# Kernel optimization log

Hardware: AMD Instinct MI355X
Metric: run time of the kernel (lower is better)

## Reference

```python
import jax, jax.numpy as jnp
import numpy as np

B, T = 512, 200
N_SKILLS, M, DK, DV, H = 1000, 50, 64, 64, 128


def setup_inputs() -> dict:
    key = jax.random.key(0)
    ks = jax.random.split(key, 12)
    inp = {
        'skill_seq': jax.random.randint(ks[0], (B, T), 0, N_SKILLS, dtype=jnp.int32),
        'correct_seq': jax.random.randint(ks[1], (B, T), 0, 2, dtype=jnp.int32),
        'mask': jnp.ones((B, T), dtype=jnp.float32),
        'skill_embed': jax.random.normal(ks[2], (N_SKILLS, DK), dtype=jnp.float32),
        'key_memory': jax.random.normal(ks[3], (M, DK), dtype=jnp.float32) * 0.1,
        'value_init': jnp.zeros((M, DV), dtype=jnp.float32),
        'interaction_embed': jax.random.normal(ks[4], (2 * N_SKILLS, DV), dtype=jnp.float32),
        'erase_W': jax.random.normal(ks[5], (DV, DV), dtype=jnp.float32) * 0.05,
        'erase_b': jnp.zeros((DV,), dtype=jnp.float32),
        'add_W': jax.random.normal(ks[6], (DV, DV), dtype=jnp.float32) * 0.05,
        'add_b': jnp.zeros((DV,), dtype=jnp.float32),
        'fc1_W': jax.random.normal(ks[7], (DK + DV, H), dtype=jnp.float32) * 0.05,
        'fc1_b': jnp.zeros((H,), dtype=jnp.float32),
        'fc2_W': jax.random.normal(ks[8], (H, 1), dtype=jnp.float32) * 0.05,
        'fc2_b': jnp.zeros((1,), dtype=jnp.float32),
    }
    return inp


def reference(skill_seq, correct_seq, mask, skill_embed, key_memory, value_init,
              interaction_embed, erase_W, erase_b, add_W, add_b,
              fc1_W, fc1_b, fc2_W, fc2_b):
    n_skills = skill_embed.shape[0]
    b = skill_seq.shape[0]
    # Time-invariant-per-step quantities are precomputed vectorized over (B,T):
    q = skill_embed[skill_seq]                                   # (B,T,dk)
    w = jax.nn.softmax(jnp.einsum('btk,mk->btm', q, key_memory), axis=-1)  # (B,T,M)
    v = interaction_embed[skill_seq + correct_seq * n_skills]    # (B,T,dv)
    e = jax.nn.sigmoid(v @ erase_W + erase_b)                    # (B,T,dv)
    a = jnp.tanh(v @ add_W + add_b)                              # (B,T,dv)

    def step(mem, inputs):
        # mem: (B,M,dv); read BEFORE write, matching the torch loop
        w_t, e_t, a_t = inputs                                   # (B,M),(B,dv),(B,dv)
        read = jnp.einsum('bm,bmv->bv', w_t, mem)                # (B,dv)
        we = w_t[:, :, None]                                     # (B,M,1)
        mem = mem * (1.0 - we * e_t[:, None, :]) + we * a_t[:, None, :]
        return mem, read

    mem0 = jnp.broadcast_to(value_init, (b,) + value_init.shape)
    _, reads = jax.lax.scan(step, mem0,
                            (jnp.swapaxes(w, 0, 1), jnp.swapaxes(e, 0, 1), jnp.swapaxes(a, 0, 1)))
    reads = jnp.swapaxes(reads, 0, 1)                            # (B,T,dv)

    x = jnp.concatenate([q, reads], axis=-1)                     # (B,T,dk+dv)
    h = jax.nn.relu(x @ fc1_W + fc1_b)
    logit = (h @ fc2_W + fc2_b)[..., 0]
    p = jax.nn.sigmoid(logit)
    return p * mask, correct_seq.astype(jnp.float32) * mask
```

## Files before the change

kernel.cpp:

```cpp
#include <hip/hip_runtime.h>
#include <hip/hip_bf16.h>

#define B_  512
#define T_  200
#define NS  1000
#define M_  50
#define DK  64
#define DV  64
#define H_  128
#define NPOS (B_ * T_)

typedef __hip_bfloat16 bf16;
typedef unsigned short ushort_t;
typedef __bf16 bf16x8 __attribute__((ext_vector_type(8)));
typedef float  f32x4  __attribute__((ext_vector_type(4)));

__device__ __forceinline__ float ldf(const void* p, int i, int isbf) {
    return isbf ? __bfloat162float(((const bf16*)p)[i]) : ((const float*)p)[i];
}
__device__ __forceinline__ int sniff(const void* mask) {
    return (*(const unsigned*)mask == 0x3F800000u) ? 0 : 1;
}
__device__ __forceinline__ float rl(float x, int l) {
    return __int_as_float(__builtin_amdgcn_readlane(__float_as_int(x), l));
}
__device__ __forceinline__ ushort_t f2bf(float v) {
    bf16 h = __float2bfloat16(v);
    return *(ushort_t*)&h;
}

__global__ __launch_bounds__(256) void dk32_tabs(
    const int*  __restrict__ cseq,
    const void* __restrict__ mask,
    const void* __restrict__ skill_embed, const void* __restrict__ key_memory,
    const void* __restrict__ inter,
    const void* __restrict__ eW, const void* __restrict__ eb,
    const void* __restrict__ aW, const void* __restrict__ ab,
    const void* __restrict__ fc1W, const void* __restrict__ fc1b,
    float* __restrict__ w_tab, unsigned* __restrict__ ea_tab,
    float* __restrict__ hq2, ushort_t* __restrict__ W2f,
    float* __restrict__ out1) {
    int isbf = sniff(mask);
    int lane = threadIdx.x & 63;
    int gwid = (blockIdx.x << 2) | (threadIdx.x >> 6);

    if (gwid < NS) {
        int s = gwid;
        float q = ldf(skill_embed, s * DK + lane, isbf);
        float acc = 0.f;
        if (lane < M_) {
            #pragma unroll 16
            for (int k = 0; k < DK; ++k)
                acc = fmaf(rl(q, k), ldf(key_memory, lane * DK + k, isbf), acc);
        }
        float val = (lane < M_) ? acc : -1e30f;
        float mx = val;
        #pragma unroll
        for (int off = 1; off < 64; off <<= 1) mx = fmaxf(mx, __shfl_xor(mx, off, 64));
        float ex = (lane < M_) ? __expf(val - mx) : 0.f;
        float sm = ex;
        #pragma unroll
        for (int off = 1; off < 64; off <<= 1) sm += __shfl_xor(sm, off, 64);
        w_tab[s * 64 + lane] = (lane < M_) ? ex / sm : 0.f;
    } else if (gwid < 3 * NS) {
        int r = gwid - NS;
        float vv = ldf(inter, r * DV + lane, isbf);
        float eacc = ldf(eb, lane, isbf);
        float aacc = ldf(ab, lane, isbf);
        #pragma unroll 16
        for (int u = 0; u < DV; ++u) {
            float vu = rl(vv, u);
            eacc = fmaf(vu, ldf(eW, u * DV + lane, isbf), eacc);
            aacc = fmaf(vu, ldf(aW, u * DV + lane, isbf), aacc);
        }
        float ev = 1.f / (1.f + __expf(-eacc));
        float av = tanhf(aacc);
        ea_tab[r * 64 + lane] = ((unsigned)f2bf(av) << 16) | (unsigned)f2bf(ev);
    } else if (gwid < 4 * NS) {
        int s = gwid - 3 * NS;
        float q = ldf(skill_embed, s * DK + lane, isbf);
        float acc0 = ldf(fc1b, lane, isbf);
        float acc1 = ldf(fc1b, 64 + lane, isbf);
        #pragma unroll 16
        for (int k = 0; k < DK; ++k) {
            float qk = rl(q, k);
            acc0 = fmaf(qk, ldf(fc1W, k * H_ + lane, isbf), acc0);
            acc1 = fmaf(qk, ldf(fc1W, k * H_ + 64 + lane, isbf), acc1);
        }
        hq2[s * H_ + (lane & 15) * 8 +     (lane >> 4)] = acc0;
        hq2[s * H_ + (lane & 15) * 8 + 4 + (lane >> 4)] = acc1;
    } else if (gwid < 4 * NS + 16) {
        int f = gwid - 4 * NS;
        int tile = f >> 1, kk = f & 1;
        int n = tile * 16 + (lane & 15);
        #pragma unroll
        for (int j = 0; j < 8; ++j) {
            int v = kk * 32 + (lane >> 4) * 8 + j;
            W2f[(f * 64 + lane) * 8 + j] = f2bf(ldf(fc1W, (DK + v) * H_ + n, isbf));
        }
    } else if (gwid < 4 * NS + 16 + 400) {
        int qp = gwid - (4 * NS + 16);
        int t0 = qp * 256;
        #pragma unroll
        for (int i = 0; i < 4; ++i) {
            int idx = t0 + i * 64 + lane;
            out1[idx] = (float)cseq[idx] * ldf(mask, idx, isbf);
        }
    }
}


#define FSCROW(W, MEM) \
    acc0 = fmaf(W.x, MEM.x, acc0); \
    acc1 = fmaf(W.y, MEM.y, acc1); \
    acc2 = fmaf(W.z, MEM.z, acc2); \
    acc3 = fmaf(W.w, MEM.w, acc3); \
    MEM.x = fmaf(-W.x, fmaf(e0, MEM.x, -a0), MEM.x); \
    MEM.y = fmaf(-W.y, fmaf(e0, MEM.y, -a0), MEM.y); \
    MEM.z = fmaf(-W.z, fmaf(e0, MEM.z, -a0), MEM.z); \
    MEM.w = fmaf(-W.w, fmaf(e0, MEM.w, -a0), MEM.w);

#define FSTEP(EAR, WARR, TP, TT) { \
    float e0 = __uint_as_float(EAR << 16); \
    float a0 = __uint_as_float(EAR & 0xFFFF0000u); \
    float acc0 = 0.f, acc1 = 0.f, acc2 = 0.f, acc3 = 0.f; \
    FSCROW(WARR[0], mem[0]) FSCROW(WARR[1], mem[1]) \
    FSCROW(WARR[2], mem[2]) FSCROW(WARR[3], mem[3]) \
    rbf[buf * 4096 + (TP) * 256 + (((k << 6) | lane) ^ (((TP) & 7) << 3))] = \
        f2bf((acc0 + acc1) + (acc2 + acc3)); \
    EAR = ea_tab[(s2 + c2 * NS) * 64 + lane]; \
    WARR[0] = w4[s2 * 16 + 4 * k + 0]; \
    WARR[1] = w4[s2 * 16 + 4 * k + 1]; \
    WARR[2] = w4[s2 * 16 + 4 * k + 2]; \
    WARR[3] = w4[s2 * 16 + 4 * k + 3]; \
    s2 = s3; c2 = c3; \
    { int tf = (TT) + 4; tf = tf < T_ ? tf : T_ - 1; \
      s3 = ss[base + tf]; c3 = cs[base + tf]; } }

__global__ __launch_bounds__(256, 2) void dk32_fused(
    const int*  __restrict__ ss, const int* __restrict__ cs,
    const void* __restrict__ mask, const void* __restrict__ value_init,
    const float* __restrict__ w_tab, const unsigned* __restrict__ ea_tab,
    const float* __restrict__ hq2, const ushort_t* __restrict__ W2f,
    const void* __restrict__ fc2W, const void* __restrict__ fc2b,
    float* __restrict__ out0) {

    __shared__ ushort_t rb[2][16][256];
    __shared__ float    xs[2][4][16];

    int isbf = sniff(mask);
    int lane = threadIdx.x & 63;
    int k    = threadIdx.x >> 6;
    int b    = blockIdx.x;
    const int base = b * T_;
    const float4* w4 = (const float4*)w_tab;
    int col = lane & 15, quad = lane >> 4;
    ushort_t* rbf = &rb[0][0][0];

    const bf16x8* B8 = (const bf16x8*)W2f;
    bf16x8 bA0 = B8[(2 * (2 * k)    ) * 64 + lane];
    bf16x8 bA1 = B8[(2 * (2 * k) + 1) * 64 + lane];
    bf16x8 bB0 = B8[(2 * (2 * k + 1)    ) * 64 + lane];
    bf16x8 bB1 = B8[(2 * (2 * k + 1) + 1) * 64 + lane];
    float f2wA = ldf(fc2W, (2 * k)     * 16 + col, isbf);
    float f2wB = ldf(fc2W, (2 * k + 1) * 16 + col, isbf);
    float f2b  = ldf(fc2b, 0, isbf);

    float4 mem[4];
    #pragma unroll
    for (int i = 0; i < 4; ++i) {
        int r = 16 * k + 4 * i;
        mem[i].x = (r + 0 < M_) ? ldf(value_init, (r + 0) * DV + lane, isbf) : 0.f;
        mem[i].y = (r + 1 < M_) ? ldf(value_init, (r + 1) * DV + lane, isbf) : 0.f;
        mem[i].z = (r + 2 < M_) ? ldf(value_init, (r + 2) * DV + lane, isbf) : 0.f;
        mem[i].w = (r + 3 < M_) ? ldf(value_init, (r + 3) * DV + lane, isbf) : 0.f;
    }

    int s2 = ss[base + 2], c2 = cs[base + 2];
    int s3 = ss[base + 3], c3 = cs[base + 3];

    float4 wa[4], wb[4];
    unsigned eaA, eaB;
    {
        int sA = ss[base], cA = cs[base];
        eaA = ea_tab[(sA + cA * NS) * 64 + lane];
        #pragma unroll
        for (int i = 0; i < 4; ++i) wa[i] = w4[sA * 16 + 4 * k + i];
        int sB = ss[base + 1], cB = cs[base + 1];
        eaB = ea_tab[(sB + cB * NS) * 64 + lane];
        #pragma unroll
        for (int i = 0; i < 4; ++i) wb[i] = w4[sB * 16 + 4 * k + i];
    }

    for (int cc = 0; cc < 13; ++cc) {
        int buf   = cc & 1;
        int p0    = cc * 16;

        FSTEP(eaA, wa, 0, p0 + 0) FSTEP(eaB, wb, 1, p0 + 1)

        int pA = p0 + quad * 4;
        int i0 = pA + 0 < T_ ? pA + 0 : T_ - 1;
        int i1 = pA + 1 < T_ ? pA + 1 : T_ - 1;
        int i2 = pA + 2 < T_ ? pA + 2 : T_ - 1;
        int i3 = pA + 3 < T_ ? pA + 3 : T_ - 1;
        int sp0 = ss[base + i0], sp1 = ss[base + i1];
        int sp2 = ss[base + i2], sp3 = ss[base + i3];

        FSTEP(eaA, wa, 2, p0 + 2) FSTEP(eaB, wb, 3, p0 + 3)

        float2 h0 = *(const float2*)(hq2 + sp0 * H_ + col * 8 + 2 * k);
        float2 h1 = *(const float2*)(hq2 + sp1 * H_ + col * 8 + 2 * k);
        float2 h2 = *(const float2*)(hq2 + sp2 * H_ + col * 8 + 2 * k);
        float2 h3 = *(const float2*)(hq2 + sp3 * H_ + col * 8 + 2 * k);

        FSTEP(eaA, wa, 4, p0 + 4) FSTEP(eaB, wb, 5, p0 + 5)
        FSTEP(eaA, wa, 6, p0 + 6) FSTEP(eaB, wb, 7, p0 + 7)
        if (cc != 12) {
            FSTEP(eaA, wa,  8, p0 +  8) FSTEP(eaB, wb,  9, p0 +  9)
            FSTEP(eaA, wa, 10, p0 + 10) FSTEP(eaB, wb, 11, p0 + 11)
            FSTEP(eaA, wa, 12, p0 + 12) FSTEP(eaB, wb, 13, p0 + 13)
            FSTEP(eaA, wa, 14, p0 + 14) FSTEP(eaB, wb, 15, p0 + 15)
        }
        __syncthreads();

        if (cc > 0 && k == 0 && lane < 16) {
            int p = base + (cc - 1) * 16 + lane;
            float xsum = xs[buf ^ 1][0][lane] + xs[buf ^ 1][1][lane]
                       + xs[buf ^ 1][2][lane] + xs[buf ^ 1][3][lane] + f2b;
            out0[p] = ldf(mask, p, isbf) / (1.f + __expf(-xsum));
        }

        {
            f32x4 cA = {0.f, 0.f, 0.f, 0.f}, cB = {0.f, 0.f, 0.f, 0.f};
            const bf16x8* A8 = (const bf16x8*)&rb[buf][0][0];
            #pragma unroll
            for (int kk = 0; kk < 8; ++kk) {
                bf16x8 av = A8[(col * 32 + kk * 4 + quad) ^ (col & 7)];
                if (kk & 1) {
                    cA = __builtin_amdgcn_mfma_f32_16x16x32_bf16(av, bA1, cA, 0, 0, 0);
                    cB = __builtin_amdgcn_mfma_f32_16x16x32_bf16(av, bB1, cB, 0, 0, 0);
                } else {
                    cA = __builtin_amdgcn_mfma_f32_16x16x32_bf16(av, bA0, cA, 0, 0, 0);
                    cB = __builtin_amdgcn_mfma_f32_16x16x32_bf16(av, bB0, cB, 0, 0, 0);
                }
            }
            float x0, x1, x2, x3, h;
            h = cA.x + h0.x; x0  = fmaxf(h, 0.f) * f2wA;
            h = cB.x + h0.y; x0 += fmaxf(h, 0.f) * f2wB;
            h = cA.y + h1.x; x1  = fmaxf(h, 0.f) * f2wA;
            h = cB.y + h1.y; x1 += fmaxf(h, 0.f) * f2wB;
            h = cA.z + h2.x; x2  = fmaxf(h, 0.f) * f2wA;
            h = cB.z + h2.y; x2 += fmaxf(h, 0.f) * f2wB;
            h = cA.w + h3.x; x3  = fmaxf(h, 0.f) * f2wA;
            h = cB.w + h3.y; x3 += fmaxf(h, 0.f) * f2wB;
            #pragma unroll
            for (int off = 1; off < 16; off <<= 1) {
                x0 += __shfl_xor(x0, off, 64);
                x1 += __shfl_xor(x1, off, 64);
                x2 += __shfl_xor(x2, off, 64);
                x3 += __shfl_xor(x3, off, 64);
            }
            if (col == 0) {
                xs[buf][k][quad * 4 + 0] = x0;
                xs[buf][k][quad * 4 + 1] = x1;
                xs[buf][k][quad * 4 + 2] = x2;
                xs[buf][k][quad * 4 + 3] = x3;
            }
        }
    }

    __syncthreads();
    if (k == 0 && lane < 16 && 192 + lane < T_) {
        int p = base + 192 + lane;
        float xsum = xs[0][0][lane] + xs[0][1][lane]
                   + xs[0][2][lane] + xs[0][3][lane] + f2b;
        out0[p] = ldf(mask, p, isbf) / (1.f + __expf(-xsum));
    }
}

extern "C" void kernel_launch(void* const* d_in, const int* in_sizes, int n_in,
                              void* d_out, int out_size, void* d_ws, size_t ws_size,
                              hipStream_t stream) {
    const int*  skill_seq   = (const int*)d_in[0];
    const int*  correct_seq = (const int*)d_in[1];
    const void* mask        = d_in[2];
    const void* skill_embed = d_in[3];
    const void* key_memory  = d_in[4];
    const void* value_init  = d_in[5];
    const void* inter       = d_in[6];
    const void* erase_W     = d_in[7];
    const void* erase_b     = d_in[8];
    const void* add_W       = d_in[9];
    const void* add_b       = d_in[10];
    const void* fc1_W       = d_in[11];
    const void* fc1_b       = d_in[12];
    const void* fc2_W       = d_in[13];
    const void* fc2_b       = d_in[14];
    float* out = (float*)d_out;

    float*    ws      = (float*)d_ws + 16;
    float*    w_tab   = ws;
    unsigned* ea_tab  = (unsigned*)(ws + 64000);
    float*    hq2     = ws + 192000;
    ushort_t* W2f     = (ushort_t*)(ws + 320000);

    dk32_tabs<<<1104, 256, 0, stream>>>(correct_seq, mask, skill_embed, key_memory,
                                        inter, erase_W, erase_b, add_W, add_b,
                                        fc1_W, fc1_b,
                                        w_tab, ea_tab, hq2, W2f,
                                        out + (size_t)NPOS);

    dk32_fused<<<B_, 256, 0, stream>>>(skill_seq, correct_seq, mask, value_init,
                                       w_tab, ea_tab, hq2, W2f, fc2_W, fc2_b,
                                       out);
}
```

Baseline: 160.8 us.

## Split memory rows across 8 waves per sequence instead of 4

Doubles the fused kernel's block size to 512 threads so each wave owns 8 memory rows rather than 16, halving per-thread register state and serial work in the recurrent step. The read buffer, partial-sum buffer and MFMA fc1 stage are restructured to match: each wave now computes one 16-column tile with a 16-step K loop, and the final reduction sums 8 wave partials. This adds more block-level sync participants and per-block LDS in exchange for shorter per-timestep critical paths and higher occupancy.

```diff
diff --git a/kernel.cpp b/kernel.cpp
--- a/kernel.cpp
+++ b/kernel.cpp
@@ -29,7 +29,7 @@
     return *(ushort_t*)&h;
 }
 
-__global__ __launch_bounds__(256) void dk32_tabs(
+__global__ __launch_bounds__(256) void dk33_tabs(
     const int*  __restrict__ cseq,
     const void* __restrict__ mask,
     const void* __restrict__ skill_embed, const void* __restrict__ key_memory,
@@ -125,19 +125,16 @@
     float a0 = __uint_as_float(EAR & 0xFFFF0000u); \
     float acc0 = 0.f, acc1 = 0.f, acc2 = 0.f, acc3 = 0.f; \
     FSCROW(WARR[0], mem[0]) FSCROW(WARR[1], mem[1]) \
-    FSCROW(WARR[2], mem[2]) FSCROW(WARR[3], mem[3]) \
-    rbf[buf * 4096 + (TP) * 256 + (((k << 6) | lane) ^ (((TP) & 7) << 3))] = \
+    rbf[buf * 8192 + (TP) * 512 + (((k << 6) | lane) ^ (((TP) & 7) << 3))] = \
         f2bf((acc0 + acc1) + (acc2 + acc3)); \
     EAR = ea_tab[(s2 + c2 * NS) * 64 + lane]; \
-    WARR[0] = w4[s2 * 16 + 4 * k + 0]; \
-    WARR[1] = w4[s2 * 16 + 4 * k + 1]; \
-    WARR[2] = w4[s2 * 16 + 4 * k + 2]; \
-    WARR[3] = w4[s2 * 16 + 4 * k + 3]; \
+    WARR[0] = w4[s2 * 16 + 2 * k + 0]; \
+    WARR[1] = w4[s2 * 16 + 2 * k + 1]; \
     s2 = s3; c2 = c3; \
     { int tf = (TT) + 4; tf = tf < T_ ? tf : T_ - 1; \
       s3 = ss[base + tf]; c3 = cs[base + tf]; } }
 
-__global__ __launch_bounds__(256, 2) void dk32_fused(
+__global__ __launch_bounds__(512, 4) void dk33_fused(
     const int*  __restrict__ ss, const int* __restrict__ cs,
     const void* __restrict__ mask, const void* __restrict__ value_init,
     const float* __restrict__ w_tab, const unsigned* __restrict__ ea_tab,
@@ -145,8 +142,8 @@
     const void* __restrict__ fc2W, const void* __restrict__ fc2b,
     float* __restrict__ out0) {
 
-    __shared__ ushort_t rb[2][16][256];
-    __shared__ float    xs[2][4][16];
+    __shared__ ushort_t rb[2][16][512];
+    __shared__ float    xs[2][8][16];
 
     int isbf = sniff(mask);
     int lane = threadIdx.x & 63;
@@ -158,18 +155,15 @@
     ushort_t* rbf = &rb[0][0][0];
 
     const bf16x8* B8 = (const bf16x8*)W2f;
-    bf16x8 bA0 = B8[(2 * (2 * k)    ) * 64 + lane];
-    bf16x8 bA1 = B8[(2 * (2 * k) + 1) * 64 + lane];
-    bf16x8 bB0 = B8[(2 * (2 * k + 1)    ) * 64 + lane];
-    bf16x8 bB1 = B8[(2 * (2 * k + 1) + 1) * 64 + lane];
-    float f2wA = ldf(fc2W, (2 * k)     * 16 + col, isbf);
-    float f2wB = ldf(fc2W, (2 * k + 1) * 16 + col, isbf);
-    float f2b  = ldf(fc2b, 0, isbf);
-
-    float4 mem[4];
+    bf16x8 bT0 = B8[(2 * k)     * 64 + lane];
+    bf16x8 bT1 = B8[(2 * k + 1) * 64 + lane];
+    float f2w = ldf(fc2W, k * 16 + col, isbf);
+    float f2b = ldf(fc2b, 0, isbf);
+
+    float4 mem[2];
     #pragma unroll
-    for (int i = 0; i < 4; ++i) {
-        int r = 16 * k + 4 * i;
+    for (int i = 0; i < 2; ++i) {
+        int r = 8 * k + 4 * i;
         mem[i].x = (r + 0 < M_) ? ldf(value_init, (r + 0) * DV + lane, isbf) : 0.f;
         mem[i].y = (r + 1 < M_) ? ldf(value_init, (r + 1) * DV + lane, isbf) : 0.f;
         mem[i].z = (r + 2 < M_) ? ldf(value_init, (r + 2) * DV + lane, isbf) : 0.f;
@@ -179,22 +173,20 @@
     int s2 = ss[base + 2], c2 = cs[base + 2];
     int s3 = ss[base + 3], c3 = cs[base + 3];
 
-    float4 wa[4], wb[4];
+    float4 wa[2], wb[2];
     unsigned eaA, eaB;
     {
         int sA = ss[base], cA = cs[base];
         eaA = ea_tab[(sA + cA * NS) * 64 + lane];
-        #pragma unroll
-        for (int i = 0; i < 4; ++i) wa[i] = w4[sA * 16 + 4 * k + i];
+        wa[0] = w4[sA * 16 + 2 * k + 0]; wa[1] = w4[sA * 16 + 2 * k + 1];
         int sB = ss[base + 1], cB = cs[base + 1];
         eaB = ea_tab[(sB + cB * NS) * 64 + lane];
-        #pragma unroll
-        for (int i = 0; i < 4; ++i) wb[i] = w4[sB * 16 + 4 * k + i];
+        wb[0] = w4[sB * 16 + 2 * k + 0]; wb[1] = w4[sB * 16 + 2 * k + 1];
     }
 
     for (int cc = 0; cc < 13; ++cc) {
-        int buf   = cc & 1;
-        int p0    = cc * 16;
+        int buf = cc & 1;
+        int p0  = cc * 16;
 
         FSTEP(eaA, wa, 0, p0 + 0) FSTEP(eaB, wb, 1, p0 + 1)
 
@@ -208,10 +200,10 @@
 
         FSTEP(eaA, wa, 2, p0 + 2) FSTEP(eaB, wb, 3, p0 + 3)
 
-        float2 h0 = *(const float2*)(hq2 + sp0 * H_ + col * 8 + 2 * k);
-        float2 h1 = *(const float2*)(hq2 + sp1 * H_ + col * 8 + 2 * k);
-        float2 h2 = *(const float2*)(hq2 + sp2 * H_ + col * 8 + 2 * k);
-        float2 h3 = *(const float2*)(hq2 + sp3 * H_ + col * 8 + 2 * k);
+        float h0 = hq2[sp0 * H_ + col * 8 + k];
+        float h1 = hq2[sp1 * H_ + col * 8 + k];
+        float h2 = hq2[sp2 * H_ + col * 8 + k];
+        float h3 = hq2[sp3 * H_ + col * 8 + k];
 
         FSTEP(eaA, wa, 4, p0 + 4) FSTEP(eaB, wb, 5, p0 + 5)
         FSTEP(eaA, wa, 6, p0 + 6) FSTEP(eaB, wb, 7, p0 + 7)
@@ -225,34 +217,28 @@
 
         if (cc > 0 && k == 0 && lane < 16) {
             int p = base + (cc - 1) * 16 + lane;
-            float xsum = xs[buf ^ 1][0][lane] + xs[buf ^ 1][1][lane]
-                       + xs[buf ^ 1][2][lane] + xs[buf ^ 1][3][lane] + f2b;
+            int b2 = buf ^ 1;
+            float xsum = xs[b2][0][lane] + xs[b2][1][lane]
+                       + xs[b2][2][lane] + xs[b2][3][lane]
+                       + xs[b2][4][lane] + xs[b2][5][lane]
+                       + xs[b2][6][lane] + xs[b2][7][lane] + f2b;
             out0[p] = ldf(mask, p, isbf) / (1.f + __expf(-xsum));
         }
 
         {
-            f32x4 cA = {0.f, 0.f, 0.f, 0.f}, cB = {0.f, 0.f, 0.f, 0.f};
+            f32x4 cT = {0.f, 0.f, 0.f, 0.f};
             const bf16x8* A8 = (const bf16x8*)&rb[buf][0][0];
             #pragma unroll
-            for (int kk = 0; kk < 8; ++kk) {
-                bf16x8 av = A8[(col * 32 + kk * 4 + quad) ^ (col & 7)];
-                if (kk & 1) {
-                    cA = __builtin_amdgcn_mfma_f32_16x16x32_bf16(av, bA1, cA, 0, 0, 0);
-                    cB = __builtin_amdgcn_mfma_f32_16x16x32_bf16(av, bB1, cB, 0, 0, 0);
-                } else {
-                    cA = __builtin_amdgcn_mfma_f32_16x16x32_bf16(av, bA0, cA, 0, 0, 0);
-                    cB = __builtin_amdgcn_mfma_f32_16x16x32_bf16(av, bB0, cB, 0, 0, 0);
-                }
+            for (int kk = 0; kk < 16; ++kk) {
+                bf16x8 av = A8[col * 64 + ((kk * 4 + quad) ^ (col & 7))];
+                cT = __builtin_amdgcn_mfma_f32_16x16x32_bf16(
+                         av, (kk & 1) ? bT1 : bT0, cT, 0, 0, 0);
             }
             float x0, x1, x2, x3, h;
-            h = cA.x + h0.x; x0  = fmaxf(h, 0.f) * f2wA;
-            h = cB.x + h0.y; x0 += fmaxf(h, 0.f) * f2wB;
-            h = cA.y + h1.x; x1  = fmaxf(h, 0.f) * f2wA;
-            h = cB.y + h1.y; x1 += fmaxf(h, 0.f) * f2wB;
-            h = cA.z + h2.x; x2  = fmaxf(h, 0.f) * f2wA;
-            h = cB.z + h2.y; x2 += fmaxf(h, 0.f) * f2wB;
-            h = cA.w + h3.x; x3  = fmaxf(h, 0.f) * f2wA;
-            h = cB.w + h3.y; x3 += fmaxf(h, 0.f) * f2wB;
+            h = cT.x + h0; x0 = fmaxf(h, 0.f) * f2w;
+            h = cT.y + h1; x1 = fmaxf(h, 0.f) * f2w;
+            h = cT.z + h2; x2 = fmaxf(h, 0.f) * f2w;
+            h = cT.w + h3; x3 = fmaxf(h, 0.f) * f2w;
             #pragma unroll
             for (int off = 1; off < 16; off <<= 1) {
                 x0 += __shfl_xor(x0, off, 64);
@@ -273,7 +259,9 @@
     if (k == 0 && lane < 16 && 192 + lane < T_) {
         int p = base + 192 + lane;
         float xsum = xs[0][0][lane] + xs[0][1][lane]
-                   + xs[0][2][lane] + xs[0][3][lane] + f2b;
+                   + xs[0][2][lane] + xs[0][3][lane]
+                   + xs[0][4][lane] + xs[0][5][lane]
+                   + xs[0][6][lane] + xs[0][7][lane] + f2b;
         out0[p] = ldf(mask, p, isbf) / (1.f + __expf(-xsum));
     }
 }
@@ -304,13 +292,13 @@
     float*    hq2     = ws + 192000;
     ushort_t* W2f     = (ushort_t*)(ws + 320000);
 
-    dk32_tabs<<<1104, 256, 0, stream>>>(correct_seq, mask, skill_embed, key_memory,
+    dk33_tabs<<<1104, 256, 0, stream>>>(correct_seq, mask, skill_embed, key_memory,
                                         inter, erase_W, erase_b, add_W, add_b,
                                         fc1_W, fc1_b,
                                         w_tab, ea_tab, hq2, W2f,
                                         out + (size_t)NPOS);
 
-    dk32_fused<<<B_, 256, 0, stream>>>(skill_seq, correct_seq, mask, value_init,
+    dk33_fused<<<B_, 512, 0, stream>>>(skill_seq, correct_seq, mask, value_init,
                                        w_tab, ea_tab, hq2, W2f, fc2_W, fc2_b,
                                        out);
 }
```

Result: slower. 194.9 us (+21.2%).
